# Optimization experiments

Hardware: AMD Instinct MI355X
Metric: run time of the kernel (lower is better)

## Reference

```python
import jax, jax.numpy as jnp
import numpy as np

N = 50000     # nodes
E = 400000    # nnz per hop matrix
K1 = 4        # K + 1 hops (K = 3)
D = 1280      # in_dim (pad_features target_dim)
H = 256       # hidden_dim


def setup_inputs() -> dict:
    key = jax.random.key(0)
    k0, k1, k2, k3, k4, k5 = jax.random.split(key, 6)
    X = jax.random.normal(k0, (N, D), dtype=jnp.float32)
    rows = jax.random.randint(k1, (K1, E), 0, N, dtype=jnp.int32)
    cols = jax.random.randint(k2, (K1, E), 0, N, dtype=jnp.int32)
    vals = jax.random.uniform(k3, (K1, E), dtype=jnp.float32)
    W = jax.random.normal(k4, (K1, D, H), dtype=jnp.float32) * 0.02
    b = jax.random.normal(k5, (K1, H), dtype=jnp.float32) * 0.02
    alpha = jnp.ones((1,), dtype=jnp.float32) * 0.25  # PReLU default init
    return {"X": X, "rows": rows, "cols": cols, "vals": vals,
            "W": W, "b": b, "alpha": alpha}


def _spmm(rows_k, cols_k, vals_k, X):
    # sparse A_k @ X: gather source rows, scale by edge values, scatter-add to dest rows
    return jax.ops.segment_sum(vals_k[:, None] * X[cols_k], rows_k, num_segments=N)


def reference(X, rows, cols, vals, W, b, alpha):
    out = jnp.zeros((N, H), dtype=X.dtype)
    for k in range(K1):  # small fixed hop count, structurally distinct matrices
        tmp = _spmm(rows[k], cols[k], vals[k], X)       # [N, D]
        out = out + tmp @ W[k] + b[k]                    # [N, H]
    # PReLU with single shared alpha
    return jnp.where(out >= 0, out, alpha * out)
```

## Files before the change

### kernel.cpp

```cpp
#include <hip/hip_runtime.h>
#include <hip/hip_bf16.h>
#include <stdint.h>

#define N_NODES 50000
#define E_EDGES 400000
#define K1H 4
#define D_IN 1280
#define H_OUT 256
#define NTOT 1024
#define MP 50176
#define CAP 128

typedef float f32x4 __attribute__((ext_vector_type(4)));
typedef short s16x8 __attribute__((ext_vector_type(8)));

#define GLOBAL_AS __attribute__((address_space(1)))
#define LDS_AS __attribute__((address_space(3)))

__device__ __forceinline__ void g2lds16(const void* g, void* l) {
    __builtin_amdgcn_global_load_lds((const GLOBAL_AS uint32_t*)g,
                                     (LDS_AS uint32_t*)l, 16, 0, 0);
}

__device__ __forceinline__ ushort f2bf(float x) {
    uint32_t u = __float_as_uint(x);
    uint32_t r = u + 0x7FFFu + ((u >> 16) & 1u);
    return (ushort)(r >> 16);
}
__device__ __forceinline__ float bf2f(ushort u) {
    return __uint_as_float(((uint32_t)u) << 16);
}

__global__ void cvtX_kernel(const float* __restrict__ X, ushort* __restrict__ Xb) {
    int i = (blockIdx.x * 256 + threadIdx.x) * 4;
    ushort4 o;
    if (i < N_NODES * D_IN) {
        const float4 v = *(const float4*)(X + i);
        o.x = f2bf(v.x); o.y = f2bf(v.y); o.z = f2bf(v.z); o.w = f2bf(v.w);
    } else {
        o.x = 0; o.y = 0; o.z = 0; o.w = 0;
    }
    *(ushort4*)(Xb + i) = o;
}

__global__ void cvtW_kernel(const float* __restrict__ W, ushort* __restrict__ WbT) {
    int o = blockIdx.x * 256 + threadIdx.x;
    if (o >= NTOT * D_IN) return;
    int n = o / D_IN, d = o - n * D_IN;
    int k = n >> 8, h = n & 255;
    WbT[o] = f2bf(W[(k * D_IN + d) * H_OUT + h]);
}

__global__ void scatter_kernel(const int* __restrict__ rows, const int* __restrict__ cols,
                               const float* __restrict__ vals, int* __restrict__ cnt,
                               int2* __restrict__ edges) {
    int i = blockIdx.x * 256 + threadIdx.x;
    if (i >= K1H * E_EDGES) return;
    int k = i / E_EDGES;
    int r = rows[i];
    int pos = atomicAdd(&cnt[r], 1);
    if (pos < CAP)
        edges[(size_t)r * CAP + pos] =
            make_int2((cols[i] << 10) | (k << 8), __float_as_int(vals[i]));
}

#define BARR() __builtin_amdgcn_s_barrier()
#define LGKM0() { asm volatile("s_waitcnt lgkmcnt(0)" ::: "memory"); \
                  __builtin_amdgcn_sched_barrier(0); }
#define VMC(N) asm volatile("s_waitcnt vmcnt(" #N ")" ::: "memory")

__global__ void __launch_bounds__(512, 2)
gemm_kernel(const ushort* __restrict__ Xb, const ushort* __restrict__ WbT,
            ushort* __restrict__ Yb) {
    __shared__ ushort lds[2][2][256 * 64];

    const int bid = blockIdx.x;
    const int xcd = bid & 7, j = bid >> 3;
    const int j2 = xcd * 98 + j;
    const int rt = j2 >> 2, ct = j2 & 3;
    const int rowBase = rt * 256, colBase = ct * 256;
    const int t = threadIdx.x;
    const int w = t >> 6, lane = t & 63;
    const int quad = lane >> 4, l16 = lane & 15;
    const int wm = w >> 2, wn = w & 3;

    f32x4 acc[8][4] = {};
    s16x8 af[4][2];
    s16x8 bfr[2][2][2];

    const int kcg = (t & 7) ^ ((t >> 3) & 7);
    const ushort* pA = Xb + (rowBase + (t >> 3)) * D_IN + kcg * 8;
    const ushort* pB = WbT + (colBase + (t >> 3) + wm * 32) * D_IN + kcg * 8;

#define STAGE_A(BUF, G, KT) { _Pragma("unroll") \
    for (int r = 0; r < 2; ++r) \
        g2lds16(pA + (r * 128 + (G) * 64) * D_IN + (KT) * 64, \
                &lds[BUF][0][(t + (G) * 512 + r * 1024) * 8]); }
#define STAGE_B(BUF, G, KT) { _Pragma("unroll") \
    for (int r = 0; r < 2; ++r) \
        g2lds16(pB + (r * 128 + (G) * 32) * D_IN + (KT) * 64, \
                &lds[BUF][1][(t + wm * 256 + (G) * 256 + r * 1024) * 8]); }
#define LDA_F(BUF, MH) { _Pragma("unroll") \
    for (int mt = 0; mt < 4; ++mt) { \
        const int m = wm * 128 + (MH) * 64 + mt * 16 + l16; \
        _Pragma("unroll") for (int ks = 0; ks < 2; ++ks) \
            af[mt][ks] = *(const s16x8*)&lds[BUF][0][(m * 8 + ((ks * 4 + quad) ^ (l16 & 7))) * 8]; } }
#define LDB_F(BUF, NH) { _Pragma("unroll") \
    for (int nt = 0; nt < 2; ++nt) { \
        const int n = wn * 64 + (NH) * 32 + nt * 16 + l16; \
        _Pragma("unroll") for (int ks = 0; ks < 2; ++ks) \
            bfr[NH][nt][ks] = *(const s16x8*)&lds[BUF][1][(n * 8 + ((ks * 4 + quad) ^ (l16 & 7))) * 8]; } }
#define MMA_Q(MH, NH) { __builtin_amdgcn_s_setprio(1); \
    _Pragma("unroll") for (int mt = 0; mt < 4; ++mt) \
        _Pragma("unroll") for (int nt = 0; nt < 2; ++nt) \
            _Pragma("unroll") for (int ks = 0; ks < 2; ++ks) \
                acc[(MH) * 4 + mt][(NH) * 2 + nt] = \
                    __builtin_amdgcn_mfma_f32_16x16x32_bf16(af[mt][ks], bfr[NH][nt][ks], \
                        acc[(MH) * 4 + mt][(NH) * 2 + nt], 0, 0, 0); \
    __builtin_amdgcn_s_setprio(0); }

    STAGE_A(0, 0, 0); STAGE_B(0, 0, 0); STAGE_A(0, 1, 0); STAGE_B(0, 1, 0);
    STAGE_A(1, 0, 1); STAGE_B(1, 0, 1);
    VMC(8);
    BARR();

#pragma unroll 1
    for (int i = 0; i < 9; ++i) {
        const int kt0 = 2 * i;
        LDA_F(0, 0); LDB_F(0, 0); STAGE_A(1, 1, kt0 + 1); VMC(6);
        BARR(); LGKM0(); MMA_Q(0, 0);
        LDB_F(0, 1); STAGE_B(1, 1, kt0 + 1);
        BARR(); LGKM0(); MMA_Q(0, 1);
        LDA_F(0, 1); STAGE_A(0, 0, kt0 + 2);
        BARR(); LGKM0(); MMA_Q(1, 0);
        STAGE_B(0, 0, kt0 + 2); VMC(8);
        BARR(); MMA_Q(1, 1);
        LDA_F(1, 0); LDB_F(1, 0); STAGE_A(0, 1, kt0 + 2); VMC(6);
        BARR(); LGKM0(); MMA_Q(0, 0);
        LDB_F(1, 1); STAGE_B(0, 1, kt0 + 2);
        BARR(); LGKM0(); MMA_Q(0, 1);
        LDA_F(1, 1); STAGE_A(1, 0, kt0 + 3);
        BARR(); LGKM0(); MMA_Q(1, 0);
        STAGE_B(1, 0, kt0 + 3); VMC(8);
        BARR(); MMA_Q(1, 1);
    }

    LDA_F(0, 0); LDB_F(0, 0); STAGE_A(1, 1, 19); VMC(6);
    BARR(); LGKM0(); MMA_Q(0, 0);
    LDB_F(0, 1); STAGE_B(1, 1, 19);
    BARR(); LGKM0(); MMA_Q(0, 1);
    LDA_F(0, 1);
    BARR(); LGKM0(); MMA_Q(1, 0);
    VMC(4);
    BARR(); MMA_Q(1, 1);
    LDA_F(1, 0); LDB_F(1, 0); VMC(0);
    BARR(); LGKM0(); MMA_Q(0, 0);
    LDB_F(1, 1);
    BARR(); LGKM0(); MMA_Q(0, 1);
    LDA_F(1, 1);
    BARR(); LGKM0(); MMA_Q(1, 0);
    MMA_Q(1, 1);

    #pragma unroll
    for (int mh = 0; mh < 2; ++mh)
      #pragma unroll
      for (int mt = 0; mt < 4; ++mt)
        #pragma unroll
        for (int nh = 0; nh < 2; ++nh)
          #pragma unroll
          for (int nt = 0; nt < 2; ++nt) {
            const int rr = rowBase + wm * 128 + mh * 64 + mt * 16 + quad * 4;
            const int cc = colBase + wn * 64 + nh * 32 + nt * 16 + l16;
            #pragma unroll
            for (int r = 0; r < 4; ++r)
                Yb[(rr + r) * NTOT + cc] = f2bf(acc[mh * 4 + mt][nh * 2 + nt][r]);
          }
}

#undef STAGE_A
#undef STAGE_B
#undef LDA_F
#undef LDB_F
#undef MMA_Q

__global__ void __launch_bounds__(256)
spmm_kernel(const int2* __restrict__ edges, const int* __restrict__ cnt,
            const ushort* __restrict__ Yb, const float* __restrict__ b,
            const float* __restrict__ alpha, float* __restrict__ out) {
    const int wid = threadIdx.x >> 6, lane = threadIdx.x & 63;
    const int row = blockIdx.x * 4 + wid;
    const int h0 = lane * 4;

    float4 acc = make_float4(0.f, 0.f, 0.f, 0.f);
    #pragma unroll
    for (int k = 0; k < K1H; ++k) {
        const float4 bb = *(const float4*)(b + k * H_OUT + h0);
        acc.x += bb.x; acc.y += bb.y; acc.z += bb.z; acc.w += bb.w;
    }

    const int2* eb = edges + (size_t)row * CAP;
    int e = cnt[row]; if (e > CAP) e = CAP;
    int j = 0;
    for (; j + 4 <= e; j += 4) {
        const int2 e0 = eb[j], e1 = eb[j + 1], e2 = eb[j + 2], e3 = eb[j + 3];
        const ushort4 y0 = *(const ushort4*)(Yb + e0.x + h0);
        const ushort4 y1 = *(const ushort4*)(Yb + e1.x + h0);
        const ushort4 y2 = *(const ushort4*)(Yb + e2.x + h0);
        const ushort4 y3 = *(const ushort4*)(Yb + e3.x + h0);
        const float v0 = __int_as_float(e0.y), v1 = __int_as_float(e1.y);
        const float v2 = __int_as_float(e2.y), v3 = __int_as_float(e3.y);
        acc.x += v0 * bf2f(y0.x) + v1 * bf2f(y1.x) + v2 * bf2f(y2.x) + v3 * bf2f(y3.x);
        acc.y += v0 * bf2f(y0.y) + v1 * bf2f(y1.y) + v2 * bf2f(y2.y) + v3 * bf2f(y3.y);
        acc.z += v0 * bf2f(y0.z) + v1 * bf2f(y1.z) + v2 * bf2f(y2.z) + v3 * bf2f(y3.z);
        acc.w += v0 * bf2f(y0.w) + v1 * bf2f(y1.w) + v2 * bf2f(y2.w) + v3 * bf2f(y3.w);
    }
    for (; j < e; ++j) {
        const int2 ed = eb[j];
        const float v = __int_as_float(ed.y);
        const ushort4 y = *(const ushort4*)(Yb + ed.x + h0);
        acc.x += v * bf2f(y.x);
        acc.y += v * bf2f(y.y);
        acc.z += v * bf2f(y.z);
        acc.w += v * bf2f(y.w);
    }

    const float a = alpha[0];
    float4 o;
    o.x = acc.x >= 0.f ? acc.x : a * acc.x;
    o.y = acc.y >= 0.f ? acc.y : a * acc.y;
    o.z = acc.z >= 0.f ? acc.z : a * acc.z;
    o.w = acc.w >= 0.f ? acc.w : a * acc.w;
    *(float4*)(out + row * H_OUT + h0) = o;
}

static inline size_t align256(size_t x) { return (x + 255) & ~(size_t)255; }

extern "C" void kernel_launch(void* const* d_in, const int* in_sizes, int n_in,
                              void* d_out, int out_size, void* d_ws, size_t ws_size,
                              hipStream_t stream) {
    const float* X     = (const float*)d_in[0];
    const int*   rows  = (const int*)d_in[1];
    const int*   cols  = (const int*)d_in[2];
    const float* vals  = (const float*)d_in[3];
    const float* W     = (const float*)d_in[4];
    const float* b     = (const float*)d_in[5];
    const float* alpha = (const float*)d_in[6];
    float* out = (float*)d_out;

    char* ws = (char*)d_ws;
    size_t off = 0;
    ushort* Xb  = (ushort*)(ws + off); off = align256(off + (size_t)MP * D_IN * 2);
    ushort* WbT = (ushort*)(ws + off); off = align256(off + (size_t)NTOT * D_IN * 2);
    ushort* Yb  = (ushort*)(ws + off); off = align256(off + (size_t)MP * NTOT * 2);
    int* cnt    = (int*)(ws + off);    off = align256(off + (size_t)N_NODES * 4);
    int2* edges = (int2*)(ws + off);   off = align256(off + (size_t)N_NODES * CAP * 8);

    hipMemsetAsync(cnt, 0, (size_t)N_NODES * 4, stream);

    cvtX_kernel<<<MP * D_IN / 4 / 256, 256, 0, stream>>>(X, Xb);
    cvtW_kernel<<<(NTOT * D_IN + 255) / 256, 256, 0, stream>>>(W, WbT);
    scatter_kernel<<<(K1H * E_EDGES + 255) / 256, 256, 0, stream>>>(rows, cols, vals, cnt, edges);
    gemm_kernel<<<196 * 4, 512, 0, stream>>>(Xb, WbT, Yb);
    spmm_kernel<<<N_NODES / 4, 256, 0, stream>>>(edges, cnt, Yb, b, alpha, out);
}
```

Measured before the change: 743.0 us.

## Restructure GEMM main loop into two-phase pipeline with fewer barriers

Reorganizes the double-buffered GEMM mainloop so each half-tile issues LDS fragment loads and global-to-LDS staging in larger groups, then runs two MMA quadrants per barrier instead of one. The prologue now stages only the first k-tile and waits for it fully, rather than prefetching part of the next tile. The intent is to cut the number of workgroup barriers and waitcnt stalls per k-iteration. In exchange, MMA work is interleaved less finely with memory traffic and the prefetch distance is shorter, which may expose more load latency.

```diff
diff --git a/kernel.cpp b/kernel.cpp
--- a/kernel.cpp
+++ b/kernel.cpp
@@ -120,46 +120,43 @@
     __builtin_amdgcn_s_setprio(0); }
 
     STAGE_A(0, 0, 0); STAGE_B(0, 0, 0); STAGE_A(0, 1, 0); STAGE_B(0, 1, 0);
-    STAGE_A(1, 0, 1); STAGE_B(1, 0, 1);
-    VMC(8);
+    VMC(0);
     BARR();
 
 #pragma unroll 1
     for (int i = 0; i < 9; ++i) {
         const int kt0 = 2 * i;
-        LDA_F(0, 0); LDB_F(0, 0); STAGE_A(1, 1, kt0 + 1); VMC(6);
-        BARR(); LGKM0(); MMA_Q(0, 0);
-        LDB_F(0, 1); STAGE_B(1, 1, kt0 + 1);
-        BARR(); LGKM0(); MMA_Q(0, 1);
-        LDA_F(0, 1); STAGE_A(0, 0, kt0 + 2);
-        BARR(); LGKM0(); MMA_Q(1, 0);
-        STAGE_B(0, 0, kt0 + 2); VMC(8);
-        BARR(); MMA_Q(1, 1);
-        LDA_F(1, 0); LDB_F(1, 0); STAGE_A(0, 1, kt0 + 2); VMC(6);
-        BARR(); LGKM0(); MMA_Q(0, 0);
-        LDB_F(1, 1); STAGE_B(0, 1, kt0 + 2);
-        BARR(); LGKM0(); MMA_Q(0, 1);
-        LDA_F(1, 1); STAGE_A(1, 0, kt0 + 3);
-        BARR(); LGKM0(); MMA_Q(1, 0);
-        STAGE_B(1, 0, kt0 + 3); VMC(8);
-        BARR(); MMA_Q(1, 1);
-    }
-
-    LDA_F(0, 0); LDB_F(0, 0); STAGE_A(1, 1, 19); VMC(6);
-    BARR(); LGKM0(); MMA_Q(0, 0);
-    LDB_F(0, 1); STAGE_B(1, 1, 19);
-    BARR(); LGKM0(); MMA_Q(0, 1);
+        LDA_F(0, 0); LDB_F(0, 0); LDB_F(0, 1);
+        STAGE_A(1, 0, kt0 + 1); STAGE_B(1, 0, kt0 + 1); STAGE_B(1, 1, kt0 + 1);
+        VMC(6);
+        BARR(); LGKM0(); MMA_Q(0, 0); MMA_Q(0, 1);
+        LDA_F(0, 1);
+        STAGE_A(1, 1, kt0 + 1);
+        VMC(2);
+        BARR(); LGKM0(); MMA_Q(1, 0); MMA_Q(1, 1);
+        LDA_F(1, 0); LDB_F(1, 0); LDB_F(1, 1);
+        STAGE_A(0, 0, kt0 + 2); STAGE_B(0, 0, kt0 + 2); STAGE_B(0, 1, kt0 + 2);
+        VMC(6);
+        BARR(); LGKM0(); MMA_Q(0, 0); MMA_Q(0, 1);
+        LDA_F(1, 1);
+        STAGE_A(0, 1, kt0 + 2);
+        VMC(2);
+        BARR(); LGKM0(); MMA_Q(1, 0); MMA_Q(1, 1);
+    }
+
+    LDA_F(0, 0); LDB_F(0, 0); LDB_F(0, 1);
+    STAGE_A(1, 0, 19); STAGE_B(1, 0, 19); STAGE_B(1, 1, 19);
+    VMC(6);
+    BARR(); LGKM0(); MMA_Q(0, 0); MMA_Q(0, 1);
     LDA_F(0, 1);
-    BARR(); LGKM0(); MMA_Q(1, 0);
-    VMC(4);
-    BARR(); MMA_Q(1, 1);
-    LDA_F(1, 0); LDB_F(1, 0); VMC(0);
-    BARR(); LGKM0(); MMA_Q(0, 0);
-    LDB_F(1, 1);
-    BARR(); LGKM0(); MMA_Q(0, 1);
+    STAGE_A(1, 1, 19);
+    VMC(2);
+    BARR(); LGKM0(); MMA_Q(1, 0); MMA_Q(1, 1);
+    LDA_F(1, 0); LDB_F(1, 0); LDB_F(1, 1);
+    VMC(0);
+    BARR(); LGKM0(); MMA_Q(0, 0); MMA_Q(0, 1);
     LDA_F(1, 1);
-    BARR(); LGKM0(); MMA_Q(1, 0);
-    MMA_Q(1, 1);
+    BARR(); LGKM0(); MMA_Q(1, 0); MMA_Q(1, 1);
 
     #pragma unroll
     for (int mh = 0; mh < 2; ++mh)
```

Measured after the change: 766.3 us. +3.1%, slower.

## Split GEMM tail into half-height tiles to balance the last wave

Applied to the files above, without the earlier changes.

The GEMM grid now uses full 256x256 tiles for the first 45056 rows and 128x256 half tiles for the remainder. The body is templated on the M fragment count, and the wait counts are adjusted accordingly. This is meant to reduce wave-quantization imbalance in the final wave across CUs. Half tiles have lower arithmetic intensity and more per-block overhead.

```diff
diff --git a/kernel.cpp b/kernel.cpp
--- a/kernel.cpp
+++ b/kernel.cpp
@@ -9,6 +9,9 @@
 #define H_OUT 256
 #define NTOT 1024
 #define MP 50176
+#define NFULL 704
+#define NHALF 160
+#define HALF_BASE 45056
 #define CAP 128
 
 typedef float f32x4 __attribute__((ext_vector_type(4)));
@@ -67,93 +70,108 @@
 #define BARR() __builtin_amdgcn_s_barrier()
 #define LGKM0() { asm volatile("s_waitcnt lgkmcnt(0)" ::: "memory"); \
                   __builtin_amdgcn_sched_barrier(0); }
-#define VMC(N) asm volatile("s_waitcnt vmcnt(" #N ")" ::: "memory")
-
-__global__ void __launch_bounds__(512, 2)
-gemm_kernel(const ushort* __restrict__ Xb, const ushort* __restrict__ WbT,
-            ushort* __restrict__ Yb) {
-    __shared__ ushort lds[2][2][256 * 64];
-
-    const int bid = blockIdx.x;
-    const int xcd = bid & 7, j = bid >> 3;
-    const int j2 = xcd * 98 + j;
-    const int rt = j2 >> 2, ct = j2 & 3;
-    const int rowBase = rt * 256, colBase = ct * 256;
-    const int t = threadIdx.x;
-    const int w = t >> 6, lane = t & 63;
-    const int quad = lane >> 4, l16 = lane & 15;
-    const int wm = w >> 2, wn = w & 3;
-
-    f32x4 acc[8][4] = {};
-    s16x8 af[4][2];
-    s16x8 bfr[2][2][2];
-
-    const int kcg = (t & 7) ^ ((t >> 3) & 7);
-    const ushort* pA = Xb + (rowBase + (t >> 3)) * D_IN + kcg * 8;
-    const ushort* pB = WbT + (colBase + (t >> 3) + wm * 32) * D_IN + kcg * 8;
-
-#define STAGE_A(BUF, G, KT) { _Pragma("unroll") \
-    for (int r = 0; r < 2; ++r) \
-        g2lds16(pA + (r * 128 + (G) * 64) * D_IN + (KT) * 64, \
-                &lds[BUF][0][(t + (G) * 512 + r * 1024) * 8]); }
+
+template<int N> __device__ __forceinline__ void vmc() {
+    if constexpr (N == 0)      asm volatile("s_waitcnt vmcnt(0)" ::: "memory");
+    else if constexpr (N == 3) asm volatile("s_waitcnt vmcnt(3)" ::: "memory");
+    else if constexpr (N == 4) asm volatile("s_waitcnt vmcnt(4)" ::: "memory");
+    else if constexpr (N == 6) asm volatile("s_waitcnt vmcnt(6)" ::: "memory");
+    else if constexpr (N == 8) asm volatile("s_waitcnt vmcnt(8)" ::: "memory");
+    else static_assert(N == 0, "unsupported vmcnt");
+}
+
+#define lA(BUF) (lds0 + ((BUF) * 2 + 0) * 16384)
+#define lB(BUF) (lds0 + ((BUF) * 2 + 1) * 16384)
+
+#define STAGE_A(BUF, G, KT) { \
+    if constexpr (MTF == 4) { \
+        _Pragma("unroll") for (int r = 0; r < 2; ++r) \
+            g2lds16(pA + ((r) * 128 + (G) * 64) * D_IN + (KT) * 64, \
+                    lA(BUF) + (t + (G) * 512 + (r) * 1024) * 8); \
+    } else { \
+        const int r64 = t >> 3, hi = (t >> 8) & 1; \
+        g2lds16(pA + ((G) * 32 + hi * 32) * D_IN + (KT) * 64, \
+                lA(BUF) + (((G) * 32 + (r64 & 31) + hi * 64) * 8 + (t & 7)) * 8); \
+    } }
 #define STAGE_B(BUF, G, KT) { _Pragma("unroll") \
     for (int r = 0; r < 2; ++r) \
-        g2lds16(pB + (r * 128 + (G) * 32) * D_IN + (KT) * 64, \
-                &lds[BUF][1][(t + wm * 256 + (G) * 256 + r * 1024) * 8]); }
+        g2lds16(pB + ((r) * 128 + (G) * 32) * D_IN + (KT) * 64, \
+                lB(BUF) + (t + wm * 256 + (G) * 256 + (r) * 1024) * 8); }
 #define LDA_F(BUF, MH) { _Pragma("unroll") \
-    for (int mt = 0; mt < 4; ++mt) { \
-        const int m = wm * 128 + (MH) * 64 + mt * 16 + l16; \
+    for (int mt = 0; mt < MTF; ++mt) { \
+        const int m = wm * (MTF * 32) + (MH) * (MTF * 16) + mt * 16 + l16; \
         _Pragma("unroll") for (int ks = 0; ks < 2; ++ks) \
-            af[mt][ks] = *(const s16x8*)&lds[BUF][0][(m * 8 + ((ks * 4 + quad) ^ (l16 & 7))) * 8]; } }
+            af[mt][ks] = *(const s16x8*)(lA(BUF) + (m * 8 + ((ks * 4 + quad) ^ (l16 & 7))) * 8); } }
 #define LDB_F(BUF, NH) { _Pragma("unroll") \
     for (int nt = 0; nt < 2; ++nt) { \
         const int n = wn * 64 + (NH) * 32 + nt * 16 + l16; \
         _Pragma("unroll") for (int ks = 0; ks < 2; ++ks) \
-            bfr[NH][nt][ks] = *(const s16x8*)&lds[BUF][1][(n * 8 + ((ks * 4 + quad) ^ (l16 & 7))) * 8]; } }
+            bfr[NH][nt][ks] = *(const s16x8*)(lB(BUF) + (n * 8 + ((ks * 4 + quad) ^ (l16 & 7))) * 8); } }
 #define MMA_Q(MH, NH) { __builtin_amdgcn_s_setprio(1); \
-    _Pragma("unroll") for (int mt = 0; mt < 4; ++mt) \
+    _Pragma("unroll") for (int mt = 0; mt < MTF; ++mt) \
         _Pragma("unroll") for (int nt = 0; nt < 2; ++nt) \
             _Pragma("unroll") for (int ks = 0; ks < 2; ++ks) \
-                acc[(MH) * 4 + mt][(NH) * 2 + nt] = \
+                acc[(MH) * MTF + mt][(NH) * 2 + nt] = \
                     __builtin_amdgcn_mfma_f32_16x16x32_bf16(af[mt][ks], bfr[NH][nt][ks], \
-                        acc[(MH) * 4 + mt][(NH) * 2 + nt], 0, 0, 0); \
+                        acc[(MH) * MTF + mt][(NH) * 2 + nt], 0, 0, 0); \
     __builtin_amdgcn_s_setprio(0); }
+
+template<int MTF>
+__device__ __forceinline__ void gemm_body(ushort* lds0,
+        const ushort* __restrict__ Xb, const ushort* __restrict__ WbT,
+        ushort* __restrict__ Yb, const int rowBase, const int colBase, const int t) {
+    constexpr int AL = MTF / 2;
+    constexpr int VA = 2 * AL + 2;
+    constexpr int VB = 2 * AL + 4;
+    constexpr int VT = AL + 2;
+
+    const int w = t >> 6, lane = t & 63;
+    const int quad = lane >> 4, l16 = lane & 15;
+    const int wm = w >> 2, wn = w & 3;
+
+    f32x4 acc[MTF * 2][4] = {};
+    s16x8 af[MTF][2];
+    s16x8 bfr[2][2][2];
+
+    const int kcg = (t & 7) ^ ((t >> 3) & 7);
+    const ushort* pA = Xb + (rowBase + (t >> 3)) * D_IN + kcg * 8;
+    const ushort* pB = WbT + (colBase + (t >> 3) + wm * 32) * D_IN + kcg * 8;
 
     STAGE_A(0, 0, 0); STAGE_B(0, 0, 0); STAGE_A(0, 1, 0); STAGE_B(0, 1, 0);
     STAGE_A(1, 0, 1); STAGE_B(1, 0, 1);
-    VMC(8);
+    vmc<VB>();
     BARR();
 
 #pragma unroll 1
     for (int i = 0; i < 9; ++i) {
         const int kt0 = 2 * i;
-        LDA_F(0, 0); LDB_F(0, 0); STAGE_A(1, 1, kt0 + 1); VMC(6);
+        LDA_F(0, 0); LDB_F(0, 0); STAGE_A(1, 1, kt0 + 1); vmc<VA>();
         BARR(); LGKM0(); MMA_Q(0, 0);
         LDB_F(0, 1); STAGE_B(1, 1, kt0 + 1);
         BARR(); LGKM0(); MMA_Q(0, 1);
         LDA_F(0, 1); STAGE_A(0, 0, kt0 + 2);
         BARR(); LGKM0(); MMA_Q(1, 0);
-        STAGE_B(0, 0, kt0 + 2); VMC(8);
+        STAGE_B(0, 0, kt0 + 2); vmc<VB>();
         BARR(); MMA_Q(1, 1);
-        LDA_F(1, 0); LDB_F(1, 0); STAGE_A(0, 1, kt0 + 2); VMC(6);
+        LDA_F(1, 0); LDB_F(1, 0); STAGE_A(0, 1, kt0 + 2); vmc<VA>();
         BARR(); LGKM0(); MMA_Q(0, 0);
         LDB_F(1, 1); STAGE_B(0, 1, kt0 + 2);
         BARR(); LGKM0(); MMA_Q(0, 1);
         LDA_F(1, 1); STAGE_A(1, 0, kt0 + 3);
         BARR(); LGKM0(); MMA_Q(1, 0);
-        STAGE_B(1, 0, kt0 + 3); VMC(8);
+        STAGE_B(1, 0, kt0 + 3); vmc<VB>();
         BARR(); MMA_Q(1, 1);
     }
 
-    LDA_F(0, 0); LDB_F(0, 0); STAGE_A(1, 1, 19); VMC(6);
+    LDA_F(0, 0); LDB_F(0, 0); STAGE_A(1, 1, 19); vmc<VA>();
     BARR(); LGKM0(); MMA_Q(0, 0);
     LDB_F(0, 1); STAGE_B(1, 1, 19);
     BARR(); LGKM0(); MMA_Q(0, 1);
     LDA_F(0, 1);
     BARR(); LGKM0(); MMA_Q(1, 0);
-    VMC(4);
+    vmc<VT>();
     BARR(); MMA_Q(1, 1);
-    LDA_F(1, 0); LDB_F(1, 0); VMC(0);
+    LDA_F(1, 0); LDB_F(1, 0); vmc<0>();
     BARR(); LGKM0(); MMA_Q(0, 0);
     LDB_F(1, 1);
     BARR(); LGKM0(); MMA_Q(0, 1);
@@ -164,17 +182,35 @@
     #pragma unroll
     for (int mh = 0; mh < 2; ++mh)
       #pragma unroll
-      for (int mt = 0; mt < 4; ++mt)
+      for (int mt = 0; mt < MTF; ++mt)
         #pragma unroll
         for (int nh = 0; nh < 2; ++nh)
           #pragma unroll
           for (int nt = 0; nt < 2; ++nt) {
-            const int rr = rowBase + wm * 128 + mh * 64 + mt * 16 + quad * 4;
+            const int rr = rowBase + wm * (MTF * 32) + mh * (MTF * 16) + mt * 16 + quad * 4;
             const int cc = colBase + wn * 64 + nh * 32 + nt * 16 + l16;
             #pragma unroll
             for (int r = 0; r < 4; ++r)
-                Yb[(rr + r) * NTOT + cc] = f2bf(acc[mh * 4 + mt][nh * 2 + nt][r]);
+                Yb[(rr + r) * NTOT + cc] = f2bf(acc[mh * MTF + mt][nh * 2 + nt][r]);
           }
+}
+
+__global__ void __launch_bounds__(512, 2)
+gemm_kernel(const ushort* __restrict__ Xb, const ushort* __restrict__ WbT,
+            ushort* __restrict__ Yb) {
+    __shared__ ushort lds[2][2][256 * 64];
+    const int bid = blockIdx.x;
+    const int t = threadIdx.x;
+    if (bid < NFULL) {
+        const int xcd = bid & 7, j = bid >> 3;
+        const int j2 = xcd * 88 + j;
+        gemm_body<4>(&lds[0][0][0], Xb, WbT, Yb, (j2 >> 2) * 256, (j2 & 3) * 256, t);
+    } else {
+        const int hb = bid - NFULL;
+        const int j2 = (hb & 7) * 20 + (hb >> 3);
+        gemm_body<2>(&lds[0][0][0], Xb, WbT, Yb,
+                     HALF_BASE + (j2 >> 2) * 128, (j2 & 3) * 256, t);
+    }
 }
 
 #undef STAGE_A
@@ -182,6 +218,8 @@
 #undef LDA_F
 #undef LDB_F
 #undef MMA_Q
+#undef lA
+#undef lB
 
 __global__ void __launch_bounds__(256)
 spmm_kernel(const int2* __restrict__ edges, const int* __restrict__ cnt,
@@ -260,6 +298,6 @@
     cvtX_kernel<<<MP * D_IN / 4 / 256, 256, 0, stream>>>(X, Xb);
     cvtW_kernel<<<(NTOT * D_IN + 255) / 256, 256, 0, stream>>>(W, WbT);
     scatter_kernel<<<(K1H * E_EDGES + 255) / 256, 256, 0, stream>>>(rows, cols, vals, cnt, edges);
-    gemm_kernel<<<196 * 4, 512, 0, stream>>>(Xb, WbT, Yb);
+    gemm_kernel<<<NFULL + NHALF, 512, 0, stream>>>(Xb, WbT, Yb);
     spmm_kernel<<<N_NODES / 4, 256, 0, stream>>>(edges, cnt, Yb, b, alpha, out);
 }
```

New measurement: 734.5 us. Within noise of the previous version (-1.1%).
